# Kernel tuning notes

Hardware: AMD Instinct MI355X
Metric: run time of the kernel (lower is better)

Reference implementation:

```python
import jax, jax.numpy as jnp
import numpy as np

B, S, E, D = 8, 2048, 1024, 128  # batch, seq (== max_span), embed_size, att_block_size


def setup_inputs() -> dict:
    key = jax.random.key(0)
    kx, kq, kk, kv = jax.random.split(key, 4)
    x = jax.random.normal(kx, (B, S, E), dtype=jnp.float32)
    # torch nn.Linear weight layout: [out_features, in_features]
    scale = 1.0 / np.sqrt(E)
    Wq = jax.random.normal(kq, (D, E), dtype=jnp.float32) * scale
    Wk = jax.random.normal(kk, (D, E), dtype=jnp.float32) * scale
    Wv = jax.random.normal(kv, (D, E), dtype=jnp.float32) * scale
    return {"x": x, "Wq": Wq, "Wk": Wk, "Wv": Wv}


def reference(x, Wq, Wk, Wv):
    # q/k/v projections: nn.Linear without bias -> x @ W.T
    q = jnp.einsum('bse,de->bsd', x, Wq)  # [B,S,D]
    k = jnp.einsum('bse,de->bsd', x, Wk)
    v = jnp.einsum('bse,de->bsd', x, Wv)

    scores = jnp.einsum('bqd,bkd->bqk', q, k)  # [B,S,S]
    # causal mask (tril): -inf above diagonal
    causal = jnp.tril(jnp.ones((S, S), dtype=bool))
    scores = jnp.where(causal, scores, -jnp.inf)
    # faithful to source: scores divided by sqrt(D) TWICE => effective 1/D
    scores = scores / jnp.float32(D)
    attn = jax.nn.softmax(scores, axis=-1)
    z = jnp.einsum('bqk,bkd->bqd', attn, v)  # [B,S,D]
    return z
```

## Files before the change

### kernel.cpp

```cpp
#include <hip/hip_runtime.h>
#include <cstdint>
#include <cstddef>

#define DEV __device__ __forceinline__

typedef float  f32x4  __attribute__((ext_vector_type(4)));
typedef __bf16 bf16x4 __attribute__((ext_vector_type(4)));
typedef __bf16 bf16x8 __attribute__((ext_vector_type(8)));

constexpr int B = 8, S = 2048, E = 1024, D = 128;
constexpr int M = B * S;

constexpr size_t WS_QKV   = (size_t)3 * M * D;
constexpr size_t WS_NEED  = (WS_QKV + (size_t)3 * D * E) * 2;

DEV int sniff_is_bf16(const uint32_t* w) {
  int lane = threadIdx.x & 63;
  uint32_t v = w[lane * 1001];
  int e = (v >> 7) & 0xff;
  unsigned long long b = __ballot(e >= 100 && e <= 140);
  return __popcll(b) >= 48;
}

DEV bf16x4 cvt4(float4 f) {
  bf16x4 r; r[0] = (__bf16)f.x; r[1] = (__bf16)f.y; r[2] = (__bf16)f.z; r[3] = (__bf16)f.w;
  return r;
}

__global__ __launch_bounds__(256) void wcast_kernel(
    const void* __restrict__ xp, const void* __restrict__ wqp,
    const void* __restrict__ wkp, const void* __restrict__ wvp,
    unsigned short* __restrict__ wbf) {
  const int is_b = sniff_is_bf16((const uint32_t*)xp);
  const int row = blockIdx.x;
  const void* src = row < 128 ? wqp : (row < 256 ? wkp : wvp);
  const int r = row & 127;
  const int t = threadIdx.x;
  if (is_b) {
    const uint2* s = (const uint2*)((const unsigned short*)src + (size_t)r * E) + t;
    *((uint2*)(wbf + (size_t)row * E) + t) = *s;
  } else {
    float4 f = *((const float4*)((const float*)src + (size_t)r * E) + t);
    *((bf16x4*)(wbf + (size_t)row * E) + t) = cvt4(f);
  }
}

__global__ __launch_bounds__(512, 2) void proj_kernel(
    const void* __restrict__ xp, const void* __restrict__ wqp,
    const void* __restrict__ wkp, const void* __restrict__ wvp,
    const unsigned short* __restrict__ wbf, const int use_wbf,
    unsigned short* __restrict__ ws) {
  __shared__ __align__(16) unsigned short lds[(64 + 384) * 72];
  unsigned short* xbuf = lds;
  unsigned short* wbuf = lds + 64 * 72;

  const int is_b = sniff_is_bf16((const uint32_t*)xp);
  const int m0 = blockIdx.x * 64;

  const int t = threadIdx.x, lane = t & 63, w = t >> 6;
  const int n15 = lane & 15, quad = lane >> 4;
  const int rg = w >> 1, cg = w & 1;

  f32x4 acc[12] = {};
  const int sr = t >> 3, sc8 = (t & 7) * 8;

  for (int it = 0; it < 16; ++it) {
    const int k0 = it * 64;
    __syncthreads();
    if (!is_b) {
      const float4* sx = (const float4*)((const float*)xp + (size_t)(m0 + sr) * E + k0 + sc8);
      *(bf16x4*)&xbuf[sr * 72 + sc8] = cvt4(sx[0]);
      *(bf16x4*)&xbuf[sr * 72 + sc8 + 4] = cvt4(sx[1]);
    } else {
      *(uint4*)&xbuf[sr * 72 + sc8] =
          *(const uint4*)((const unsigned short*)xp + (size_t)(m0 + sr) * E + k0 + sc8);
    }
    if (use_wbf) {
#pragma unroll
      for (int j = 0; j < 6; ++j)
        *(uint4*)&wbuf[(j * 64 + sr) * 72 + sc8] =
            *(const uint4*)(wbf + (size_t)(j * 64 + sr) * E + k0 + sc8);
    } else if (!is_b) {
#pragma unroll
      for (int j = 0; j < 6; ++j) {
        const float* wsrc = (j < 2) ? (const float*)wqp : (j < 4) ? (const float*)wkp : (const float*)wvp;
        const int wrow = (j & 1) * 64 + sr;
        const float4* sw = (const float4*)(wsrc + (size_t)wrow * E + k0 + sc8);
        *(bf16x4*)&wbuf[(j * 64 + sr) * 72 + sc8] = cvt4(sw[0]);
        *(bf16x4*)&wbuf[(j * 64 + sr) * 72 + sc8 + 4] = cvt4(sw[1]);
      }
    } else {
#pragma unroll
      for (int j = 0; j < 6; ++j) {
        const unsigned short* wsrc = (j < 2) ? (const unsigned short*)wqp
                                   : (j < 4) ? (const unsigned short*)wkp
                                             : (const unsigned short*)wvp;
        const int wrow = (j & 1) * 64 + sr;
        *(uint4*)&wbuf[(j * 64 + sr) * 72 + sc8] =
            *(const uint4*)(wsrc + (size_t)wrow * E + k0 + sc8);
      }
    }
    __syncthreads();
#pragma unroll
    for (int ks = 0; ks < 2; ++ks) {
      bf16x8 a = *(const bf16x8*)&xbuf[(rg * 16 + n15) * 72 + ks * 32 + quad * 8];
#pragma unroll
      for (int nf = 0; nf < 12; ++nf) {
        bf16x8 bfr = *(const bf16x8*)&wbuf[(cg * 192 + nf * 16 + n15) * 72 + ks * 32 + quad * 8];
        acc[nf] = __builtin_amdgcn_mfma_f32_16x16x32_bf16(a, bfr, acc[nf], 0, 0, 0);
      }
    }
  }

  unsigned short* qws = ws;
  unsigned short* kws = ws + (size_t)M * D;
  unsigned short* vtw = ws + (size_t)2 * M * D;

  __syncthreads();
  unsigned short* tbuf = lds;
#pragma unroll
  for (int nf = 0; nf < 12; ++nf) {
    const int col = cg * 192 + nf * 16 + n15;
    const int self = col >> 7;
    if (self < 2) {
      unsigned short* dst = self ? kws : qws;
      const int gcol = col & 127;
#pragma unroll
      for (int rr = 0; rr < 4; ++rr) {
        const int grow = m0 + rg * 16 + quad * 4 + rr;
        ((__bf16*)dst)[(size_t)grow * D + gcol] = (__bf16)acc[nf][rr];
      }
    } else {
      const int vcol = col - 256;
#pragma unroll
      for (int rr = 0; rr < 4; ++rr)
        ((__bf16*)tbuf)[(rg * 16 + quad * 4 + rr) * 132 + vcol] = (__bf16)acc[nf][rr];
    }
  }
  __syncthreads();
  {
    const int dcol = t >> 2, mst = (t & 3) * 16;
    unsigned short tmp[16] __attribute__((aligned(16)));
#pragma unroll
    for (int j = 0; j < 16; ++j) tmp[j] = tbuf[(mst + j) * 132 + dcol];
    *(uint4*)&vtw[(size_t)dcol * M + m0 + mst] = *(const uint4*)&tmp[0];
    *(uint4*)&vtw[(size_t)dcol * M + m0 + mst + 8] = *(const uint4*)&tmp[8];
  }
}

__global__ __launch_bounds__(256, 3) void attn_kernel(
    const void* __restrict__ xp, const unsigned short* __restrict__ ws,
    void* __restrict__ outp) {
  __shared__ __align__(16) unsigned short ldsP[4 * 1280];
  __shared__ __align__(16) float Obuf[32 * 132];
  __shared__ float lbuf[32];
  __shared__ int cnt;

  const int is_b = sniff_is_bf16((const uint32_t*)xp);
  const int bx = blockIdx.x;
  const int batch = bx & 7, t16 = 63 - (bx >> 3);
  const int q0 = t16 * 32;
  const int t = threadIdx.x, lane = t & 63, s = t >> 6;
  const int n15 = lane & 15, quad = lane >> 4;

  const unsigned short* qws = ws;
  const unsigned short* kws = ws + (size_t)M * D;
  const unsigned short* vtw = ws + (size_t)2 * M * D;
  unsigned short* ldsPw = ldsP + s * 1280;

  if (t == 0) cnt = 0;
  __syncthreads();

  bf16x8 qf[2][4];
#pragma unroll
  for (int g = 0; g < 2; ++g) {
    const size_t qbase = (size_t)(batch * S + q0 + g * 16 + n15) * D;
#pragma unroll
    for (int ks = 0; ks < 4; ++ks)
      qf[g][ks] = *(const bf16x8*)&qws[qbase + ks * 32 + quad * 8];
  }

  const bf16x8 ones = {(__bf16)1.0f, (__bf16)1.0f, (__bf16)1.0f, (__bf16)1.0f,
                       (__bf16)1.0f, (__bf16)1.0f, (__bf16)1.0f, (__bf16)1.0f};

  f32x4 o[2][8] = {};
  f32x4 lacc[2] = {};

  const int nch = (t16 + 4) >> 2;
  for (int c = 0; c < nch; ++c) {
    const int j0 = c * 128 + s * 32;

    uint4 kraw[8];
#pragma unroll
    for (int nt = 0; nt < 2; ++nt)
#pragma unroll
      for (int ks = 0; ks < 4; ++ks)
        kraw[nt * 4 + ks] = *(const uint4*)&kws[(size_t)(batch * S + j0 + nt * 16 + n15) * D + ks * 32 + quad * 8];

    f32x4 sc[2][2] = {};
#pragma unroll
    for (int ks = 0; ks < 4; ++ks)
#pragma unroll
      for (int nt = 0; nt < 2; ++nt) {
        const bf16x8 ka = *(const bf16x8*)&kraw[nt * 4 + ks];
#pragma unroll
        for (int g = 0; g < 2; ++g)
          sc[g][nt] = __builtin_amdgcn_mfma_f32_16x16x32_bf16(ka, qf[g][ks], sc[g][nt], 0, 0, 0);
      }

    const bool lastc = (c == nch - 1);
#pragma unroll
    for (int g = 0; g < 2; ++g)
#pragma unroll
      for (int nt = 0; nt < 2; ++nt) {
        bf16x4 pv;
#pragma unroll
        for (int rr = 0; rr < 4; ++rr) {
          float v = sc[g][nt][rr] * (1.0f / 128.0f);
          if (lastc && (j0 + nt * 16 + quad * 4 + rr > q0 + g * 16 + n15)) v = -1e30f;
          pv[rr] = (__bf16)__expf(v);
        }
        *(bf16x4*)&ldsPw[g * 640 + n15 * 40 + nt * 16 + quad * 4] = pv;
      }
    asm volatile("" ::: "memory");

    uint4 vraw[8];
#pragma unroll
    for (int dn = 0; dn < 8; ++dn)
      vraw[dn] = *(const uint4*)&vtw[(size_t)(dn * 16 + n15) * M + batch * S + j0 + quad * 8];

#pragma unroll
    for (int g = 0; g < 2; ++g) {
      const bf16x8 pa = *(const bf16x8*)&ldsPw[g * 640 + n15 * 40 + quad * 8];
#pragma unroll
      for (int dn = 0; dn < 8; ++dn)
        o[g][dn] = __builtin_amdgcn_mfma_f32_16x16x32_bf16(pa, *(const bf16x8*)&vraw[dn], o[g][dn], 0, 0, 0);
      lacc[g] = __builtin_amdgcn_mfma_f32_16x16x32_bf16(pa, ones, lacc[g], 0, 0, 0);
    }
  }

  if (s == 0) {
#pragma unroll
    for (int g = 0; g < 2; ++g)
#pragma unroll
      for (int dn = 0; dn < 8; ++dn)
#pragma unroll
        for (int rr = 0; rr < 4; ++rr)
          Obuf[(g * 16 + quad * 4 + rr) * 132 + dn * 16 + n15] = o[g][dn][rr];
    if (n15 == 0)
#pragma unroll
      for (int g = 0; g < 2; ++g)
#pragma unroll
        for (int rr = 0; rr < 4; ++rr)
          lbuf[g * 16 + quad * 4 + rr] = lacc[g][rr];
    asm volatile("" ::: "memory");
    if (lane == 0) atomicAdd(&cnt, 1);
  } else {
    while (__hip_atomic_load(&cnt, __ATOMIC_RELAXED, __HIP_MEMORY_SCOPE_WORKGROUP) < 1)
      __builtin_amdgcn_s_sleep(1);
    asm volatile("" ::: "memory");
#pragma unroll
    for (int g = 0; g < 2; ++g)
#pragma unroll
      for (int dn = 0; dn < 8; ++dn)
#pragma unroll
        for (int rr = 0; rr < 4; ++rr)
          atomicAdd(&Obuf[(g * 16 + quad * 4 + rr) * 132 + dn * 16 + n15], o[g][dn][rr]);
    if (n15 == 0)
#pragma unroll
      for (int g = 0; g < 2; ++g)
#pragma unroll
        for (int rr = 0; rr < 4; ++rr)
          atomicAdd(&lbuf[g * 16 + quad * 4 + rr], lacc[g][rr]);
    if (lane == 0) atomicAdd(&cnt, 1);
  }
  while (__hip_atomic_load(&cnt, __ATOMIC_RELAXED, __HIP_MEMORY_SCOPE_WORKGROUP) < 4)
    __builtin_amdgcn_s_sleep(1);
  asm volatile("" ::: "memory");

  {
    const int row = t >> 3, cb = (t & 7) * 16;
    const float invl = 1.0f / lbuf[row];
    const size_t grow = (size_t)(batch * S + q0 + row) * D;
    if (is_b) {
#pragma unroll
      for (int i = 0; i < 16; ++i)
        ((__bf16*)outp)[grow + cb + i] = (__bf16)(Obuf[row * 132 + cb + i] * invl);
    } else {
#pragma unroll
      for (int i = 0; i < 16; ++i)
        ((float*)outp)[grow + cb + i] = Obuf[row * 132 + cb + i] * invl;
    }
  }
}

extern "C" void kernel_launch(void* const* d_in, const int* in_sizes, int n_in,
                              void* d_out, int out_size, void* d_ws, size_t ws_size,
                              hipStream_t stream) {
  (void)in_sizes; (void)n_in; (void)out_size;
  const void* x  = d_in[0];
  const void* wq = d_in[1];
  const void* wk = d_in[2];
  const void* wv = d_in[3];
  unsigned short* ws = (unsigned short*)d_ws;
  unsigned short* wbf = ws + WS_QKV;
  const int use_wbf = (ws_size >= WS_NEED) ? 1 : 0;

  if (use_wbf)
    wcast_kernel<<<dim3(384), dim3(256), 0, stream>>>(x, wq, wk, wv, wbf);
  proj_kernel<<<dim3(256), dim3(512), 0, stream>>>(x, wq, wk, wv, wbf, use_wbf, ws);
  attn_kernel<<<dim3(512), dim3(256), 0, stream>>>(x, ws, d_out);
}
```

Measured before the change: 193.2 us.

## Split attention block into two 16-row query groups across 8 waves

The attention kernel now runs 512 threads per block. Each of the 8 waves handles one 16-row query group and one quarter of the key chunk, instead of 4 waves each covering both 32-row groups. This halves per-wave register state and doubles the number of waves available to hide latency. Waves whose key chunk lies entirely above the causal diagonal for their query group now skip it. In exchange, each K/V tile is loaded twice per block (once per query group), and the reduction uses per-group counters and spin-waits across 8 waves.

```diff
diff --git a/kernel.cpp b/kernel.cpp
--- a/kernel.cpp
+++ b/kernel.cpp
@@ -148,80 +148,74 @@
   }
 }
 
-__global__ __launch_bounds__(256, 3) void attn_kernel(
+__global__ __launch_bounds__(512, 4) void attn_kernel(
     const void* __restrict__ xp, const unsigned short* __restrict__ ws,
     void* __restrict__ outp) {
-  __shared__ __align__(16) unsigned short ldsP[4 * 1280];
+  __shared__ __align__(16) unsigned short ldsP[8 * 640];
   __shared__ __align__(16) float Obuf[32 * 132];
   __shared__ float lbuf[32];
-  __shared__ int cnt;
+  __shared__ int cnt2[2];
 
   const int is_b = sniff_is_bf16((const uint32_t*)xp);
   const int bx = blockIdx.x;
   const int batch = bx & 7, t16 = 63 - (bx >> 3);
   const int q0 = t16 * 32;
   const int t = threadIdx.x, lane = t & 63, s = t >> 6;
+  const int kq = s & 3, qg = s >> 2;
   const int n15 = lane & 15, quad = lane >> 4;
 
   const unsigned short* qws = ws;
   const unsigned short* kws = ws + (size_t)M * D;
   const unsigned short* vtw = ws + (size_t)2 * M * D;
-  unsigned short* ldsPw = ldsP + s * 1280;
-
-  if (t == 0) cnt = 0;
+  unsigned short* ldsPw = ldsP + s * 640;
+
+  if (t < 2) cnt2[t] = 0;
   __syncthreads();
 
-  bf16x8 qf[2][4];
-#pragma unroll
-  for (int g = 0; g < 2; ++g) {
-    const size_t qbase = (size_t)(batch * S + q0 + g * 16 + n15) * D;
+  bf16x8 qf[4];
+  {
+    const size_t qbase = (size_t)(batch * S + q0 + qg * 16 + n15) * D;
 #pragma unroll
     for (int ks = 0; ks < 4; ++ks)
-      qf[g][ks] = *(const bf16x8*)&qws[qbase + ks * 32 + quad * 8];
+      qf[ks] = *(const bf16x8*)&qws[qbase + ks * 32 + quad * 8];
   }
 
   const bf16x8 ones = {(__bf16)1.0f, (__bf16)1.0f, (__bf16)1.0f, (__bf16)1.0f,
                        (__bf16)1.0f, (__bf16)1.0f, (__bf16)1.0f, (__bf16)1.0f};
 
-  f32x4 o[2][8] = {};
-  f32x4 lacc[2] = {};
-
+  f32x4 o[8] = {};
+  f32x4 lacc = {};
+
+  const int qmax = q0 + qg * 16 + 15;
   const int nch = (t16 + 4) >> 2;
   for (int c = 0; c < nch; ++c) {
-    const int j0 = c * 128 + s * 32;
-
-    uint4 kraw[8];
-#pragma unroll
-    for (int nt = 0; nt < 2; ++nt)
+    const int j0 = c * 128 + kq * 32;
+    if (j0 > qmax) continue;
+
+    f32x4 sc[2] = {};
+#pragma unroll
+    for (int nt = 0; nt < 2; ++nt) {
+      uint4 kraw[4];
 #pragma unroll
       for (int ks = 0; ks < 4; ++ks)
-        kraw[nt * 4 + ks] = *(const uint4*)&kws[(size_t)(batch * S + j0 + nt * 16 + n15) * D + ks * 32 + quad * 8];
-
-    f32x4 sc[2][2] = {};
-#pragma unroll
-    for (int ks = 0; ks < 4; ++ks)
-#pragma unroll
-      for (int nt = 0; nt < 2; ++nt) {
-        const bf16x8 ka = *(const bf16x8*)&kraw[nt * 4 + ks];
-#pragma unroll
-        for (int g = 0; g < 2; ++g)
-          sc[g][nt] = __builtin_amdgcn_mfma_f32_16x16x32_bf16(ka, qf[g][ks], sc[g][nt], 0, 0, 0);
-      }
+        kraw[ks] = *(const uint4*)&kws[(size_t)(batch * S + j0 + nt * 16 + n15) * D + ks * 32 + quad * 8];
+#pragma unroll
+      for (int ks = 0; ks < 4; ++ks)
+        sc[nt] = __builtin_amdgcn_mfma_f32_16x16x32_bf16(*(const bf16x8*)&kraw[ks], qf[ks], sc[nt], 0, 0, 0);
+    }
 
     const bool lastc = (c == nch - 1);
 #pragma unroll
-    for (int g = 0; g < 2; ++g)
-#pragma unroll
-      for (int nt = 0; nt < 2; ++nt) {
-        bf16x4 pv;
-#pragma unroll
-        for (int rr = 0; rr < 4; ++rr) {
-          float v = sc[g][nt][rr] * (1.0f / 128.0f);
-          if (lastc && (j0 + nt * 16 + quad * 4 + rr > q0 + g * 16 + n15)) v = -1e30f;
-          pv[rr] = (__bf16)__expf(v);
-        }
-        *(bf16x4*)&ldsPw[g * 640 + n15 * 40 + nt * 16 + quad * 4] = pv;
-      }
+    for (int nt = 0; nt < 2; ++nt) {
+      bf16x4 pv;
+#pragma unroll
+      for (int rr = 0; rr < 4; ++rr) {
+        float v = sc[nt][rr] * (1.0f / 128.0f);
+        if (lastc && (j0 + nt * 16 + quad * 4 + rr > q0 + qg * 16 + n15)) v = -1e30f;
+        pv[rr] = (__bf16)__expf(v);
+      }
+      *(bf16x4*)&ldsPw[n15 * 40 + nt * 16 + quad * 4] = pv;
+    }
     asm volatile("" ::: "memory");
 
     uint4 vraw[8];
@@ -229,66 +223,56 @@
     for (int dn = 0; dn < 8; ++dn)
       vraw[dn] = *(const uint4*)&vtw[(size_t)(dn * 16 + n15) * M + batch * S + j0 + quad * 8];
 
-#pragma unroll
-    for (int g = 0; g < 2; ++g) {
-      const bf16x8 pa = *(const bf16x8*)&ldsPw[g * 640 + n15 * 40 + quad * 8];
-#pragma unroll
-      for (int dn = 0; dn < 8; ++dn)
-        o[g][dn] = __builtin_amdgcn_mfma_f32_16x16x32_bf16(pa, *(const bf16x8*)&vraw[dn], o[g][dn], 0, 0, 0);
-      lacc[g] = __builtin_amdgcn_mfma_f32_16x16x32_bf16(pa, ones, lacc[g], 0, 0, 0);
-    }
-  }
-
-  if (s == 0) {
-#pragma unroll
-    for (int g = 0; g < 2; ++g)
-#pragma unroll
-      for (int dn = 0; dn < 8; ++dn)
-#pragma unroll
-        for (int rr = 0; rr < 4; ++rr)
-          Obuf[(g * 16 + quad * 4 + rr) * 132 + dn * 16 + n15] = o[g][dn][rr];
+    const bf16x8 pa = *(const bf16x8*)&ldsPw[n15 * 40 + quad * 8];
+#pragma unroll
+    for (int dn = 0; dn < 8; ++dn)
+      o[dn] = __builtin_amdgcn_mfma_f32_16x16x32_bf16(pa, *(const bf16x8*)&vraw[dn], o[dn], 0, 0, 0);
+    lacc = __builtin_amdgcn_mfma_f32_16x16x32_bf16(pa, ones, lacc, 0, 0, 0);
+  }
+
+  if (kq == 0) {
+#pragma unroll
+    for (int dn = 0; dn < 8; ++dn)
+#pragma unroll
+      for (int rr = 0; rr < 4; ++rr)
+        Obuf[(qg * 16 + quad * 4 + rr) * 132 + dn * 16 + n15] = o[dn][rr];
     if (n15 == 0)
 #pragma unroll
-      for (int g = 0; g < 2; ++g)
-#pragma unroll
-        for (int rr = 0; rr < 4; ++rr)
-          lbuf[g * 16 + quad * 4 + rr] = lacc[g][rr];
+      for (int rr = 0; rr < 4; ++rr)
+        lbuf[qg * 16 + quad * 4 + rr] = lacc[rr];
     asm volatile("" ::: "memory");
-    if (lane == 0) atomicAdd(&cnt, 1);
+    if (lane == 0) atomicAdd(&cnt2[qg], 1);
   } else {
-    while (__hip_atomic_load(&cnt, __ATOMIC_RELAXED, __HIP_MEMORY_SCOPE_WORKGROUP) < 1)
+    while (__hip_atomic_load(&cnt2[qg], __ATOMIC_RELAXED, __HIP_MEMORY_SCOPE_WORKGROUP) < 1)
       __builtin_amdgcn_s_sleep(1);
     asm volatile("" ::: "memory");
 #pragma unroll
-    for (int g = 0; g < 2; ++g)
-#pragma unroll
-      for (int dn = 0; dn < 8; ++dn)
-#pragma unroll
-        for (int rr = 0; rr < 4; ++rr)
-          atomicAdd(&Obuf[(g * 16 + quad * 4 + rr) * 132 + dn * 16 + n15], o[g][dn][rr]);
+    for (int dn = 0; dn < 8; ++dn)
+#pragma unroll
+      for (int rr = 0; rr < 4; ++rr)
+        atomicAdd(&Obuf[(qg * 16 + quad * 4 + rr) * 132 + dn * 16 + n15], o[dn][rr]);
     if (n15 == 0)
 #pragma unroll
-      for (int g = 0; g < 2; ++g)
-#pragma unroll
-        for (int rr = 0; rr < 4; ++rr)
-          atomicAdd(&lbuf[g * 16 + quad * 4 + rr], lacc[g][rr]);
-    if (lane == 0) atomicAdd(&cnt, 1);
-  }
-  while (__hip_atomic_load(&cnt, __ATOMIC_RELAXED, __HIP_MEMORY_SCOPE_WORKGROUP) < 4)
+      for (int rr = 0; rr < 4; ++rr)
+        atomicAdd(&lbuf[qg * 16 + quad * 4 + rr], lacc[rr]);
+    if (lane == 0) atomicAdd(&cnt2[qg], 1);
+  }
+  while (__hip_atomic_load(&cnt2[0], __ATOMIC_RELAXED, __HIP_MEMORY_SCOPE_WORKGROUP) < 4 ||
+         __hip_atomic_load(&cnt2[1], __ATOMIC_RELAXED, __HIP_MEMORY_SCOPE_WORKGROUP) < 4)
     __builtin_amdgcn_s_sleep(1);
   asm volatile("" ::: "memory");
 
   {
-    const int row = t >> 3, cb = (t & 7) * 16;
+    const int row = t >> 4, cb = (t & 15) * 8;
     const float invl = 1.0f / lbuf[row];
     const size_t grow = (size_t)(batch * S + q0 + row) * D;
     if (is_b) {
 #pragma unroll
-      for (int i = 0; i < 16; ++i)
+      for (int i = 0; i < 8; ++i)
         ((__bf16*)outp)[grow + cb + i] = (__bf16)(Obuf[row * 132 + cb + i] * invl);
     } else {
 #pragma unroll
-      for (int i = 0; i < 16; ++i)
+      for (int i = 0; i < 8; ++i)
         ((float*)outp)[grow + cb + i] = Obuf[row * 132 + cb + i] * invl;
     }
   }
@@ -309,5 +293,5 @@
   if (use_wbf)
     wcast_kernel<<<dim3(384), dim3(256), 0, stream>>>(x, wq, wk, wv, wbf);
   proj_kernel<<<dim3(256), dim3(512), 0, stream>>>(x, wq, wk, wv, wbf, use_wbf, ws);
-  attn_kernel<<<dim3(512), dim3(256), 0, stream>>>(x, ws, d_out);
-}
+  attn_kernel<<<dim3(512), dim3(512), 0, stream>>>(x, ws, d_out);
+}
```

Result: slower. 229.6 us (+18.9%).

## Prefetch next K tile, skip fully-masked key chunks per wave, reorder block schedule

Applied to the files above, without the earlier changes.

The attention loop now loads the next chunk's K fragments into registers while the current chunk's score MFMAs run, and issues the V loads earlier in the iteration. Each wave computes its own chunk count so it skips key chunks lying entirely above the causal diagonal. The block-to-tile mapping is changed so the second half of the grid runs tiles in ascending order, and launch bounds are relaxed from 3 to 2 blocks per SM to leave more registers for the prefetch buffers. The risk is lower occupancy and a possible mismatch between the new grid mapping and the launch size.

```diff
diff --git a/kernel.cpp b/kernel.cpp
--- a/kernel.cpp
+++ b/kernel.cpp
@@ -148,7 +148,7 @@
   }
 }
 
-__global__ __launch_bounds__(256, 3) void attn_kernel(
+__global__ __launch_bounds__(256, 2) void attn_kernel(
     const void* __restrict__ xp, const unsigned short* __restrict__ ws,
     void* __restrict__ outp) {
   __shared__ __align__(16) unsigned short ldsP[4 * 1280];
@@ -158,9 +158,12 @@
 
   const int is_b = sniff_is_bf16((const uint32_t*)xp);
   const int bx = blockIdx.x;
-  const int batch = bx & 7, t16 = 63 - (bx >> 3);
+  const int batch = bx & 7;
+  const int g8 = (bx & 255) >> 3;
+  const int t16 = (bx < 256) ? (63 - g8) : g8;
   const int q0 = t16 * 32;
   const int t = threadIdx.x, lane = t & 63, s = t >> 6;
+  const int kq = s;
   const int n15 = lane & 15, quad = lane >> 4;
 
   const unsigned short* qws = ws;
@@ -187,54 +190,82 @@
   f32x4 lacc[2] = {};
 
   const int nch = (t16 + 4) >> 2;
-  for (int c = 0; c < nch; ++c) {
-    const int j0 = c * 128 + s * 32;
-
-    uint4 kraw[8];
+  const int ncw = (t16 >= kq) ? (((((t16 - kq) << 5) + 31) >> 7) + 1) : 0;
+
+  uint4 kr[8], vr[8];
+
+  const size_t kbase = (size_t)(batch * S) * D;
+  const size_t vbase = (size_t)batch * S;
+
+  if (ncw > 0) {
+    const int j0 = kq * 32;
 #pragma unroll
     for (int nt = 0; nt < 2; ++nt)
 #pragma unroll
       for (int ks = 0; ks < 4; ++ks)
-        kraw[nt * 4 + ks] = *(const uint4*)&kws[(size_t)(batch * S + j0 + nt * 16 + n15) * D + ks * 32 + quad * 8];
+        kr[nt * 4 + ks] = *(const uint4*)&kws[kbase + (size_t)(j0 + nt * 16 + n15) * D + ks * 32 + quad * 8];
+  }
+
+  for (int c = 0; c < ncw; ++c) {
+    const int j0 = c * 128 + kq * 32;
+
+#pragma unroll
+    for (int dn = 0; dn < 8; ++dn)
+      vr[dn] = *(const uint4*)&vtw[(size_t)(dn * 16 + n15) * M + vbase + j0 + quad * 8];
 
     f32x4 sc[2][2] = {};
 #pragma unroll
     for (int ks = 0; ks < 4; ++ks)
 #pragma unroll
       for (int nt = 0; nt < 2; ++nt) {
-        const bf16x8 ka = *(const bf16x8*)&kraw[nt * 4 + ks];
+        const bf16x8 ka = *(const bf16x8*)&kr[nt * 4 + ks];
 #pragma unroll
         for (int g = 0; g < 2; ++g)
           sc[g][nt] = __builtin_amdgcn_mfma_f32_16x16x32_bf16(ka, qf[g][ks], sc[g][nt], 0, 0, 0);
       }
 
-    const bool lastc = (c == nch - 1);
-#pragma unroll
-    for (int g = 0; g < 2; ++g)
-#pragma unroll
-      for (int nt = 0; nt < 2; ++nt) {
-        bf16x4 pv;
-#pragma unroll
-        for (int rr = 0; rr < 4; ++rr) {
-          float v = sc[g][nt][rr] * (1.0f / 128.0f);
-          if (lastc && (j0 + nt * 16 + quad * 4 + rr > q0 + g * 16 + n15)) v = -1e30f;
-          pv[rr] = (__bf16)__expf(v);
+    if (c + 1 < ncw) {
+      const int j1 = j0 + 128;
+#pragma unroll
+      for (int nt = 0; nt < 2; ++nt)
+#pragma unroll
+        for (int ks = 0; ks < 4; ++ks)
+          kr[nt * 4 + ks] = *(const uint4*)&kws[kbase + (size_t)(j1 + nt * 16 + n15) * D + ks * 32 + quad * 8];
+    }
+
+    if (c == nch - 1) {
+#pragma unroll
+      for (int g = 0; g < 2; ++g)
+#pragma unroll
+        for (int nt = 0; nt < 2; ++nt) {
+          bf16x4 pv;
+#pragma unroll
+          for (int rr = 0; rr < 4; ++rr) {
+            float v = sc[g][nt][rr] * (1.0f / 128.0f);
+            if (j0 + nt * 16 + quad * 4 + rr > q0 + g * 16 + n15) v = -1e30f;
+            pv[rr] = (__bf16)__expf(v);
+          }
+          *(bf16x4*)&ldsPw[g * 640 + n15 * 40 + nt * 16 + quad * 4] = pv;
         }
-        *(bf16x4*)&ldsPw[g * 640 + n15 * 40 + nt * 16 + quad * 4] = pv;
-      }
-    asm volatile("" ::: "memory");
-
-    uint4 vraw[8];
-#pragma unroll
-    for (int dn = 0; dn < 8; ++dn)
-      vraw[dn] = *(const uint4*)&vtw[(size_t)(dn * 16 + n15) * M + batch * S + j0 + quad * 8];
+    } else {
+#pragma unroll
+      for (int g = 0; g < 2; ++g)
+#pragma unroll
+        for (int nt = 0; nt < 2; ++nt) {
+          bf16x4 pv;
+#pragma unroll
+          for (int rr = 0; rr < 4; ++rr)
+            pv[rr] = (__bf16)__expf(sc[g][nt][rr] * (1.0f / 128.0f));
+          *(bf16x4*)&ldsPw[g * 640 + n15 * 40 + nt * 16 + quad * 4] = pv;
+        }
+    }
 
 #pragma unroll
     for (int g = 0; g < 2; ++g) {
       const bf16x8 pa = *(const bf16x8*)&ldsPw[g * 640 + n15 * 40 + quad * 8];
 #pragma unroll
       for (int dn = 0; dn < 8; ++dn)
-        o[g][dn] = __builtin_amdgcn_mfma_f32_16x16x32_bf16(pa, *(const bf16x8*)&vraw[dn], o[g][dn], 0, 0, 0);
+        o[g][dn] = __builtin_amdgcn_mfma_f32_16x16x32_bf16(pa, *(const bf16x8*)&vr[dn], o[g][dn], 0, 0, 0);
       lacc[g] = __builtin_amdgcn_mfma_f32_16x16x32_bf16(pa, ones, lacc[g], 0, 0, 0);
     }
   }
```

Result: no change. 190.6 us (-1.3%).

## Stage K/V tiles in LDS with double-buffered direct global-to-LDS loads, 64-row query tiles

Applied to the files above, without the earlier changes.

The attention kernel now handles 64 query rows per block instead of 32, which halves the grid to 256 blocks. K and V^T tiles of 128 keys are copied straight into a swizzled, double-buffered LDS area with global_load_lds, so the next chunk's load overlaps compute on the current one. Each wave reads its 32-key slice from LDS and reuses it across four row groups, which cuts repeated global reads. In exchange, occupancy drops to one block per CU with a large LDS footprint, and a block barrier is added per chunk. Causal load balance also changes, since block index no longer maps heavy tiles first.

```diff
diff --git a/kernel.cpp b/kernel.cpp
--- a/kernel.cpp
+++ b/kernel.cpp
@@ -25,6 +25,12 @@
 DEV bf16x4 cvt4(float4 f) {
   bf16x4 r; r[0] = (__bf16)f.x; r[1] = (__bf16)f.y; r[2] = (__bf16)f.z; r[3] = (__bf16)f.w;
   return r;
+}
+
+DEV void glds16(const void* g, void* l) {
+  __builtin_amdgcn_global_load_lds(
+      (const __attribute__((address_space(1))) void*)g,
+      (__attribute__((address_space(3))) void*)l, 16, 0, 0);
 }
 
 __global__ __launch_bounds__(256) void wcast_kernel(
@@ -148,111 +154,159 @@
   }
 }
 
-__global__ __launch_bounds__(256, 3) void attn_kernel(
+__global__ __launch_bounds__(256, 1) void attn_kernel(
     const void* __restrict__ xp, const unsigned short* __restrict__ ws,
     void* __restrict__ outp) {
-  __shared__ __align__(16) unsigned short ldsP[4 * 1280];
-  __shared__ __align__(16) float Obuf[32 * 132];
-  __shared__ float lbuf[32];
+  __shared__ __align__(16) unsigned short kvbuf[2 * 32768];
+  __shared__ __align__(16) unsigned short ldsP[4 * 2560];
+  __shared__ float lbuf[64];
   __shared__ int cnt;
 
   const int is_b = sniff_is_bf16((const uint32_t*)xp);
   const int bx = blockIdx.x;
-  const int batch = bx & 7, t16 = 63 - (bx >> 3);
-  const int q0 = t16 * 32;
+  const int batch = bx & 7, T = bx >> 3;
+  const int q0 = T * 64;
   const int t = threadIdx.x, lane = t & 63, s = t >> 6;
+  const int kq = s;
   const int n15 = lane & 15, quad = lane >> 4;
 
   const unsigned short* qws = ws;
   const unsigned short* kws = ws + (size_t)M * D;
   const unsigned short* vtw = ws + (size_t)2 * M * D;
-  unsigned short* ldsPw = ldsP + s * 1280;
+  unsigned short* ldsPw = ldsP + s * 2560;
 
   if (t == 0) cnt = 0;
-  __syncthreads();
-
-  bf16x8 qf[2][4];
-#pragma unroll
-  for (int g = 0; g < 2; ++g) {
-    const size_t qbase = (size_t)(batch * S + q0 + g * 16 + n15) * D;
+
+  bf16x8 qf[4][4];
+#pragma unroll
+  for (int rg = 0; rg < 4; ++rg) {
+    const size_t qbase = (size_t)(batch * S + q0 + rg * 16 + n15) * D;
 #pragma unroll
     for (int ks = 0; ks < 4; ++ks)
-      qf[g][ks] = *(const bf16x8*)&qws[qbase + ks * 32 + quad * 8];
+      qf[rg][ks] = *(const bf16x8*)&qws[qbase + ks * 32 + quad * 8];
   }
 
   const bf16x8 ones = {(__bf16)1.0f, (__bf16)1.0f, (__bf16)1.0f, (__bf16)1.0f,
                        (__bf16)1.0f, (__bf16)1.0f, (__bf16)1.0f, (__bf16)1.0f};
 
-  f32x4 o[2][8] = {};
-  f32x4 lacc[2] = {};
-
-  const int nch = (t16 + 4) >> 2;
+  f32x4 o[4][8] = {};
+  f32x4 lacc[4] = {};
+
+  const int nch = (T + 2) >> 1;
+  const int ncw = (q0 + 63 >= kq * 32) ? (((q0 + 63 - kq * 32) >> 7) + 1) : 0;
+
+  const int r4 = lane >> 4, c16 = lane & 15;
+  const size_t kgbase = (size_t)(batch * S) * D;
+  const size_t vgbase = (size_t)batch * S;
+
+  {
+    unsigned short* kb = kvbuf;
+    unsigned short* vb = kvbuf + 16384;
+#pragma unroll
+    for (int i = 0; i < 8; ++i) {
+      const int key = s * 32 + i * 4 + r4;
+      glds16(kws + kgbase + (size_t)key * D + ((c16 ^ (key & 7)) << 3),
+             kb + (s * 32 + i * 4) * 128);
+    }
+#pragma unroll
+    for (int i = 0; i < 8; ++i) {
+      const int dr = s * 32 + i * 4 + r4;
+      glds16(vtw + (size_t)dr * M + vgbase + ((c16 ^ (dr & 7)) << 3),
+             vb + (s * 32 + i * 4) * 128);
+    }
+  }
+  __syncthreads();
+
   for (int c = 0; c < nch; ++c) {
-    const int j0 = c * 128 + s * 32;
-
-    uint4 kraw[8];
-#pragma unroll
-    for (int nt = 0; nt < 2; ++nt)
-#pragma unroll
-      for (int ks = 0; ks < 4; ++ks)
-        kraw[nt * 4 + ks] = *(const uint4*)&kws[(size_t)(batch * S + j0 + nt * 16 + n15) * D + ks * 32 + quad * 8];
-
-    f32x4 sc[2][2] = {};
-#pragma unroll
-    for (int ks = 0; ks < 4; ++ks)
+    const unsigned short* kb = kvbuf + (c & 1) * 32768;
+    const unsigned short* vb = kb + 16384;
+
+    if (c + 1 < nch) {
+      unsigned short* kb2 = kvbuf + ((c + 1) & 1) * 32768;
+      unsigned short* vb2 = kb2 + 16384;
+      const int j1 = (c + 1) * 128;
+#pragma unroll
+      for (int i = 0; i < 8; ++i) {
+        const int key = s * 32 + i * 4 + r4;
+        glds16(kws + kgbase + (size_t)(j1 + key) * D + ((c16 ^ (key & 7)) << 3),
+               kb2 + (s * 32 + i * 4) * 128);
+      }
+#pragma unroll
+      for (int i = 0; i < 8; ++i) {
+        const int dr = s * 32 + i * 4 + r4;
+        glds16(vtw + (size_t)dr * M + vgbase + j1 + ((c16 ^ (dr & 7)) << 3),
+               vb2 + (s * 32 + i * 4) * 128);
+      }
+    }
+
+    if (c < ncw) {
+      const int j0 = c * 128 + kq * 32;
+      const int xsw = (n15 & 7);
+
+      f32x4 sc[4][2] = {};
 #pragma unroll
       for (int nt = 0; nt < 2; ++nt) {
-        const bf16x8 ka = *(const bf16x8*)&kraw[nt * 4 + ks];
-#pragma unroll
-        for (int g = 0; g < 2; ++g)
-          sc[g][nt] = __builtin_amdgcn_mfma_f32_16x16x32_bf16(ka, qf[g][ks], sc[g][nt], 0, 0, 0);
-      }
-
-    const bool lastc = (c == nch - 1);
-#pragma unroll
-    for (int g = 0; g < 2; ++g)
-#pragma unroll
-      for (int nt = 0; nt < 2; ++nt) {
-        bf16x4 pv;
-#pragma unroll
-        for (int rr = 0; rr < 4; ++rr) {
-          float v = sc[g][nt][rr] * (1.0f / 128.0f);
-          if (lastc && (j0 + nt * 16 + quad * 4 + rr > q0 + g * 16 + n15)) v = -1e30f;
-          pv[rr] = (__bf16)__expf(v);
+        const int klrow = kq * 32 + nt * 16 + n15;
+#pragma unroll
+        for (int ks = 0; ks < 4; ++ks) {
+          const bf16x8 ka =
+              *(const bf16x8*)&kb[klrow * 128 + (((ks * 4 + quad) ^ xsw) << 3)];
+#pragma unroll
+          for (int rg = 0; rg < 4; ++rg)
+            sc[rg][nt] = __builtin_amdgcn_mfma_f32_16x16x32_bf16(ka, qf[rg][ks], sc[rg][nt], 0, 0, 0);
         }
-        *(bf16x4*)&ldsPw[g * 640 + n15 * 40 + nt * 16 + quad * 4] = pv;
-      }
-    asm volatile("" ::: "memory");
-
-    uint4 vraw[8];
-#pragma unroll
-    for (int dn = 0; dn < 8; ++dn)
-      vraw[dn] = *(const uint4*)&vtw[(size_t)(dn * 16 + n15) * M + batch * S + j0 + quad * 8];
-
-#pragma unroll
-    for (int g = 0; g < 2; ++g) {
-      const bf16x8 pa = *(const bf16x8*)&ldsPw[g * 640 + n15 * 40 + quad * 8];
+      }
+
+      const bool maskc = (c == ncw - 1);
+#pragma unroll
+      for (int rg = 0; rg < 4; ++rg)
+#pragma unroll
+        for (int nt = 0; nt < 2; ++nt) {
+          bf16x4 pv;
+#pragma unroll
+          for (int rr = 0; rr < 4; ++rr) {
+            float v = sc[rg][nt][rr] * (1.0f / 128.0f);
+            if (maskc && (j0 + nt * 16 + quad * 4 + rr > q0 + rg * 16 + n15)) v = -1e30f;
+            pv[rr] = (__bf16)__expf(v);
+          }
+          *(bf16x4*)&ldsPw[rg * 640 + n15 * 40 + nt * 16 + quad * 4] = pv;
+        }
+
+      bf16x8 pa[4];
+#pragma unroll
+      for (int rg = 0; rg < 4; ++rg)
+        pa[rg] = *(const bf16x8*)&ldsPw[rg * 640 + n15 * 40 + quad * 8];
+#pragma unroll
+      for (int dn = 0; dn < 8; ++dn) {
+        const bf16x8 vfr =
+            *(const bf16x8*)&vb[(dn * 16 + n15) * 128 + ((((kq * 4 + quad) ^ xsw)) << 3)];
+#pragma unroll
+        for (int rg = 0; rg < 4; ++rg)
+          o[rg][dn] = __builtin_amdgcn_mfma_f32_16x16x32_bf16(pa[rg], vfr, o[rg][dn], 0, 0, 0);
+      }
+#pragma unroll
+      for (int rg = 0; rg < 4; ++rg)
+        lacc[rg] = __builtin_amdgcn_mfma_f32_16x16x32_bf16(pa[rg], ones, lacc[rg], 0, 0, 0);
+    }
+
+    __syncthreads();
+  }
+
+  float* Obuf = (float*)kvbuf;
+  if (s == 0) {
+#pragma unroll
+    for (int rg = 0; rg < 4; ++rg)
 #pragma unroll
       for (int dn = 0; dn < 8; ++dn)
-        o[g][dn] = __builtin_amdgcn_mfma_f32_16x16x32_bf16(pa, *(const bf16x8*)&vraw[dn], o[g][dn], 0, 0, 0);
-      lacc[g] = __builtin_amdgcn_mfma_f32_16x16x32_bf16(pa, ones, lacc[g], 0, 0, 0);
-    }
-  }
-
-  if (s == 0) {
-#pragma unroll
-    for (int g = 0; g < 2; ++g)
-#pragma unroll
-      for (int dn = 0; dn < 8; ++dn)
 #pragma unroll
         for (int rr = 0; rr < 4; ++rr)
-          Obuf[(g * 16 + quad * 4 + rr) * 132 + dn * 16 + n15] = o[g][dn][rr];
+          Obuf[(rg * 16 + quad * 4 + rr) * 132 + dn * 16 + n15] = o[rg][dn][rr];
     if (n15 == 0)
 #pragma unroll
-      for (int g = 0; g < 2; ++g)
+      for (int rg = 0; rg < 4; ++rg)
 #pragma unroll
         for (int rr = 0; rr < 4; ++rr)
-          lbuf[g * 16 + quad * 4 + rr] = lacc[g][rr];
+          lbuf[rg * 16 + quad * 4 + rr] = lacc[rg][rr];
     asm volatile("" ::: "memory");
     if (lane == 0) atomicAdd(&cnt, 1);
   } else {
@@ -260,18 +314,18 @@
       __builtin_amdgcn_s_sleep(1);
     asm volatile("" ::: "memory");
 #pragma unroll
-    for (int g = 0; g < 2; ++g)
+    for (int rg = 0; rg < 4; ++rg)
 #pragma unroll
       for (int dn = 0; dn < 8; ++dn)
 #pragma unroll
         for (int rr = 0; rr < 4; ++rr)
-          atomicAdd(&Obuf[(g * 16 + quad * 4 + rr) * 132 + dn * 16 + n15], o[g][dn][rr]);
+          atomicAdd(&Obuf[(rg * 16 + quad * 4 + rr) * 132 + dn * 16 + n15], o[rg][dn][rr]);
     if (n15 == 0)
 #pragma unroll
-      for (int g = 0; g < 2; ++g)
+      for (int rg = 0; rg < 4; ++rg)
 #pragma unroll
         for (int rr = 0; rr < 4; ++rr)
-          atomicAdd(&lbuf[g * 16 + quad * 4 + rr], lacc[g][rr]);
+          atomicAdd(&lbuf[rg * 16 + quad * 4 + rr], lacc[rg][rr]);
     if (lane == 0) atomicAdd(&cnt, 1);
   }
   while (__hip_atomic_load(&cnt, __ATOMIC_RELAXED, __HIP_MEMORY_SCOPE_WORKGROUP) < 4)
@@ -279,16 +333,16 @@
   asm volatile("" ::: "memory");
 
   {
-    const int row = t >> 3, cb = (t & 7) * 16;
+    const int row = t >> 2, cb = (t & 3) * 32;
     const float invl = 1.0f / lbuf[row];
     const size_t grow = (size_t)(batch * S + q0 + row) * D;
     if (is_b) {
 #pragma unroll
-      for (int i = 0; i < 16; ++i)
+      for (int i = 0; i < 32; ++i)
         ((__bf16*)outp)[grow + cb + i] = (__bf16)(Obuf[row * 132 + cb + i] * invl);
     } else {
 #pragma unroll
-      for (int i = 0; i < 16; ++i)
+      for (int i = 0; i < 32; ++i)
         ((float*)outp)[grow + cb + i] = Obuf[row * 132 + cb + i] * invl;
     }
   }
@@ -309,5 +363,5 @@
   if (use_wbf)
     wcast_kernel<<<dim3(384), dim3(256), 0, stream>>>(x, wq, wk, wv, wbf);
   proj_kernel<<<dim3(256), dim3(512), 0, stream>>>(x, wq, wk, wv, wbf, use_wbf, ws);
-  attn_kernel<<<dim3(512), dim3(256), 0, stream>>>(x, ws, d_out);
-}
+  attn_kernel<<<dim3(256), dim3(256), 0, stream>>>(x, ws, d_out);
+}
```

New measurement: 206.9 us. +7.1%, slower.
